# Optimization experiments

Measured on AMD Instinct MI355X. Metric: run time of the kernel, lower is better.

## Reference

```python
import jax, jax.numpy as jnp
import numpy as np

NEG_INF = -1e30
LRELU_SLOPE = 0.2

B, E, IN_DIM, OUT_DIM = 64, 512, 1024, 256


def setup_inputs() -> dict:
    key = jax.random.key(0)
    ks = jax.random.split(key, 6)
    input_state = jax.random.normal(ks[0], (B, E, IN_DIM), dtype=jnp.float32)
    adj = jnp.ones((B, E, E), dtype=jnp.float32)  # only used via ones_like in the original
    node_mask = jax.random.randint(ks[1], (B, E, 1), 0, 2, dtype=jnp.int32)
    W_w = jax.random.normal(ks[2], (OUT_DIM, IN_DIM), dtype=jnp.float32) * (1.0 / np.sqrt(IN_DIM))
    W_b = jax.random.normal(ks[3], (OUT_DIM,), dtype=jnp.float32) * 0.02
    a_w = jax.random.normal(ks[4], (1, 2 * OUT_DIM), dtype=jnp.float32) * (1.0 / np.sqrt(2 * OUT_DIM))
    a_b = jax.random.normal(ks[5], (1,), dtype=jnp.float32) * 0.02
    return {"input_state": input_state, "adj": adj, "node_mask": node_mask,
            "W_w": W_w, "W_b": W_b, "a_w": a_w, "a_b": a_b}


def reference(input_state, adj, node_mask, W_w, W_b, a_w, a_b):
    # h = W(input_state); dropout is identity in eval mode (gnn_drop=0)
    h = jnp.einsum('bei,oi->beo', input_state, W_w) + W_b  # b,E,d
    d = h.shape[-1]
    # a([h_i ; h_j]) decomposes exactly: a_w[:, :d] @ h_i + a_w[:, d:] @ h_j + a_b
    a1, a2 = a_w[:, :d], a_w[:, d:]
    s1 = jnp.einsum('beo,xo->bex', h, a1)  # b,E,1 -> score contribution of source node i
    s2 = jnp.einsum('beo,xo->bex', h, a2)  # b,E,1 -> contribution of target node j
    scores = s1 + jnp.swapaxes(s2, 1, 2) + a_b  # b,E,E, scores[n,i,j] = a([h_i;h_j])
    scores = jnp.where(scores >= 0, scores, LRELU_SLOPE * scores)  # LeakyReLU(0.2)
    # fully-connected adjacency gated by node mask: mask_i * mask_j
    m = node_mask.astype(scores.dtype)  # b,E,1
    pair_mask = m * jnp.swapaxes(m, 1, 2)  # b,E,E
    scores = jnp.where(pair_mask > 0, scores, NEG_INF)
    coefs = jax.nn.softmax(scores, axis=-1)  # b,E,E
    h = h * m  # zero out masked nodes before aggregation
    return jnp.einsum('bij,bjo->bio', coefs, h)
```

## Files before the change

kernel.cpp:

```cpp
#include <hip/hip_runtime.h>
#include <hip/hip_fp16.h>
#include <math.h>

#define NEG_INF_F (-1e30f)
#define LRELU 0.2f

constexpr int Bb = 64, Ee = 512, IND = 1024, OUTD = 256;
constexpr int Mrows = Bb * Ee;

typedef __attribute__((ext_vector_type(8))) _Float16 half8;
typedef __attribute__((ext_vector_type(4))) _Float16 half4;
typedef __attribute__((ext_vector_type(4))) float floatx4;

#define AS1 __attribute__((address_space(1)))
#define AS3 __attribute__((address_space(3)))

__global__ __launch_bounds__(256) void wconv_kernel(
    const float* __restrict__ W, _Float16* __restrict__ Whf)
{
    const int i = (blockIdx.x * 256 + threadIdx.x) * 4;
    const float4 w = *reinterpret_cast<const float4*>(&W[i]);
    half4 hh;
    hh[0] = (_Float16)w.x; hh[1] = (_Float16)w.y;
    hh[2] = (_Float16)w.z; hh[3] = (_Float16)w.w;
    *reinterpret_cast<half4*>(&Whf[i]) = hh;
}

__global__ __launch_bounds__(256, 2) void gemm_h_f16(
    const float* __restrict__ X, const _Float16* __restrict__ Whf,
    const float* __restrict__ Wb, const float* __restrict__ aw,
    const int* __restrict__ mask,
    _Float16* __restrict__ HmTh, float* __restrict__ s1, float* __restrict__ s2)
{
    __shared__ char lds_raw[73728];
    float*    Af  = (float*)lds_raw;
    _Float16* Bf  = (_Float16*)(lds_raw + 24576);
    _Float16* Th   = (_Float16*)lds_raw;
    float*    s1p  = (float*)(lds_raw + 32768);
    float*    s2p  = (float*)(lds_raw + 33792);
    float*    mkfs = (float*)(lds_raw + 34816);

    const int t  = threadIdx.x;
    const int w  = t >> 6, l = t & 63, ln = l & 15, lg = l >> 4;
    const int m0 = blockIdx.x * 64;

    const int arl = l >> 3;
    const int agl = (l & 7) ^ arl;
    const int brl = l >> 2;
    const int bgl = (l & 3) ^ ((l >> 3) & 3);

    floatx4 acc[4][4];
    #pragma unroll
    for (int i = 0; i < 4; ++i)
        #pragma unroll
        for (int j = 0; j < 4; ++j)
            acc[i][j] = (floatx4)0.f;

    auto stageA = [&](int kc, int aoff) {
        #pragma unroll
        for (int i = 0; i < 2; ++i) {
            const int rbase = (w * 2 + i) * 8;
            const size_t src = (size_t)(m0 + rbase + arl) * IND + kc * 32 + agl * 4;
            __builtin_amdgcn_global_load_lds(
                (const AS1 unsigned int*)(X + src),
                (AS3 unsigned int*)(Af + aoff + rbase * 32), 16, 0, 0);
        }
    };
    auto stageB = [&](int kc, int boff) {
        #pragma unroll
        for (int i = 0; i < 4; ++i) {
            const int nbase = w * 64 + i * 16;
            const size_t src = (size_t)(nbase + brl) * IND + kc * 32 + bgl * 8;
            __builtin_amdgcn_global_load_lds(
                (const AS1 unsigned int*)(Whf + src),
                (AS3 unsigned int*)(Bf + boff + nbase * 32), 16, 0, 0);
        }
    };

    int aO0 = 0, aO1 = 2048, aO2 = 4096;
    int bO0 = 0, bO1 = 8192, bO2 = 16384;

    stageA(0, aO0); stageB(0, bO0);
    stageA(1, aO1); stageB(1, bO1);
    asm volatile("s_waitcnt vmcnt(6) lgkmcnt(0)" ::: "memory");
    __builtin_amdgcn_sched_barrier(0);
    __builtin_amdgcn_s_barrier();
    __builtin_amdgcn_sched_barrier(0);

    for (int ts = 0; ts < 32; ++ts) {
        if (ts < 30) { stageA(ts + 2, aO2); stageB(ts + 2, bO2); }
        __builtin_amdgcn_sched_barrier(0);

        half8 bfrag[4];
        #pragma unroll
        for (int nr = 0; nr < 4; ++nr) {
            const int n = w * 64 + nr * 16 + ln;
            const int phys = lg ^ ((n >> 1) & 3);
            bfrag[nr] = *reinterpret_cast<const half8*>(Bf + bO0 + n * 32 + phys * 8);
        }
        half8 afrag[4];
        #pragma unroll
        for (int mr = 0; mr < 4; ++mr) {
            const int r = mr * 16 + ln;
            const int g0 = (lg * 2) ^ (r & 7);
            const int g1 = (lg * 2 + 1) ^ (r & 7);
            const floatx4 a0 = *reinterpret_cast<const floatx4*>(Af + aO0 + r * 32 + g0 * 4);
            const floatx4 a1 = *reinterpret_cast<const floatx4*>(Af + aO0 + r * 32 + g1 * 4);
            half8 h;
            h[0] = (_Float16)a0[0]; h[1] = (_Float16)a0[1];
            h[2] = (_Float16)a0[2]; h[3] = (_Float16)a0[3];
            h[4] = (_Float16)a1[0]; h[5] = (_Float16)a1[1];
            h[6] = (_Float16)a1[2]; h[7] = (_Float16)a1[3];
            afrag[mr] = h;
        }

        __builtin_amdgcn_s_setprio(1);
        #pragma unroll
        for (int mr = 0; mr < 4; ++mr)
            #pragma unroll
            for (int nr = 0; nr < 4; ++nr)
                acc[mr][nr] = __builtin_amdgcn_mfma_f32_16x16x32_f16(
                    afrag[mr], bfrag[nr], acc[mr][nr], 0, 0, 0);
        __builtin_amdgcn_s_setprio(0);

        if (ts < 29) asm volatile("s_waitcnt vmcnt(6) lgkmcnt(0)" ::: "memory");
        else         asm volatile("s_waitcnt vmcnt(0) lgkmcnt(0)" ::: "memory");
        __builtin_amdgcn_sched_barrier(0);
        __builtin_amdgcn_s_barrier();
        __builtin_amdgcn_sched_barrier(0);

        int tmp = aO0; aO0 = aO1; aO1 = aO2; aO2 = tmp;
        tmp = bO0; bO0 = bO1; bO1 = bO2; bO2 = tmp;
    }

    if (t < 64) mkfs[t] = (float)mask[m0 + t];

    float bias[4], a1c[4], a2c[4];
    #pragma unroll
    for (int nr = 0; nr < 4; ++nr) {
        const int n = w * 64 + nr * 16 + ln;
        bias[nr] = Wb[n];
        a1c[nr]  = aw[n];
        a2c[nr]  = aw[OUTD + n];
    }
    float sv1[4][4], sv2[4][4];
    #pragma unroll
    for (int i = 0; i < 4; ++i)
        #pragma unroll
        for (int r = 0; r < 4; ++r) { sv1[i][r] = 0.f; sv2[i][r] = 0.f; }

    #pragma unroll
    for (int mr = 0; mr < 4; ++mr)
        #pragma unroll
        for (int nr = 0; nr < 4; ++nr) {
            const int o = w * 64 + nr * 16 + ln;
            half4 hh;
            #pragma unroll
            for (int rr = 0; rr < 4; ++rr) {
                const float hb = acc[mr][nr][rr] + bias[nr];
                sv1[mr][rr] += hb * a1c[nr];
                sv2[mr][rr] += hb * a2c[nr];
                hh[rr] = (_Float16)hb;
            }
            const int e = mr * 16 + lg * 4;
            *reinterpret_cast<half4*>(Th + o * 64 + (e ^ ((o & 7) << 3))) = hh;
        }

    #pragma unroll
    for (int mr = 0; mr < 4; ++mr)
        #pragma unroll
        for (int rr = 0; rr < 4; ++rr) {
            float v1 = sv1[mr][rr], v2 = sv2[mr][rr];
            #pragma unroll
            for (int off = 1; off < 16; off <<= 1) {
                v1 += __shfl_xor(v1, off, 64);
                v2 += __shfl_xor(v2, off, 64);
            }
            if (ln == 0) {
                const int e = mr * 16 + lg * 4 + rr;
                s1p[w * 64 + e] = v1;
                s2p[w * 64 + e] = v2;
            }
        }
    __syncthreads();

    if (t < 64) {
        s1[m0 + t] = s1p[t] + s1p[64 + t] + s1p[128 + t] + s1p[192 + t];
        s2[m0 + t] = s2p[t] + s2p[64 + t] + s2p[128 + t] + s2p[192 + t];
    }

    const int bIdx = m0 >> 9;
    const int e0   = m0 & 511;
    const int e4   = (t & 15) * 4;
    const float q0 = mkfs[e4 + 0], q1 = mkfs[e4 + 1];
    const float q2 = mkfs[e4 + 2], q3 = mkfs[e4 + 3];
    #pragma unroll
    for (int it = 0; it < 16; ++it) {
        const int o = it * 16 + (t >> 4);
        half4 vh = *reinterpret_cast<const half4*>(Th + o * 64 + (e4 ^ ((o & 7) << 3)));
        if (!(q0 > 0.f)) vh[0] = (_Float16)0.f;
        if (!(q1 > 0.f)) vh[1] = (_Float16)0.f;
        if (!(q2 > 0.f)) vh[2] = (_Float16)0.f;
        if (!(q3 > 0.f)) vh[3] = (_Float16)0.f;
        const size_t goff = ((size_t)(bIdx * OUTD + o) << 9) + e0 + e4;
        *reinterpret_cast<half4*>(&HmTh[goff]) = vh;
    }
}

__global__ __launch_bounds__(256, 2) void attn_mfma(
    const _Float16* __restrict__ HmTh,
    const float* __restrict__ s1, const float* __restrict__ s2,
    const int* __restrict__ mask, const float* __restrict__ ab_ptr,
    float* __restrict__ Out)
{
    __shared__ float s2v[Ee];
    __shared__ float mkv[Ee];
    __shared__ float rowc[64];
    __shared__ float rmax[64];
    __shared__ int   rvv[64];
    __shared__ _Float16 Pl[2][64][32];
    __shared__ float Zp[64][4];
    __shared__ float zr[64];
    __shared__ float wmax[4];

    const int bid = blockIdx.x;
    const int b  = bid & 63;
    const int i0 = (bid >> 6) * 64;
    const int t  = threadIdx.x;
    const int w  = t >> 6, l = t & 63, ln = l & 15, lg = l >> 4;
    const float ab = ab_ptr[0];

    float lmax = -INFINITY;
    #pragma unroll
    for (int q = 0; q < 2; ++q) {
        const int j = t + q * 256;
        const float sv = s2[b * Ee + j];
        const float mv = (float)mask[b * Ee + j];
        s2v[j] = sv; mkv[j] = mv;
        if (mv > 0.f) lmax = fmaxf(lmax, sv);
    }
    #pragma unroll
    for (int off = 32; off; off >>= 1) lmax = fmaxf(lmax, __shfl_xor(lmax, off, 64));
    if (l == 0) wmax[w] = lmax;
    __syncthreads();
    const float s2max = fmaxf(fmaxf(wmax[0], wmax[1]), fmaxf(wmax[2], wmax[3]));
    const int anyvalid = (s2max > -1e37f) ? 1 : 0;
    if (t < 64) {
        const float c = s1[b * Ee + i0 + t] + ab;
        rowc[t] = c;
        const int mi = mask[b * Ee + i0 + t];
        rvv[t] = (mi != 0) & anyvalid;
        const float rm = c + s2max;
        rmax[t] = (rm >= 0.f) ? rm : LRELU * rm;
    }
    __syncthreads();

    const int pi = t >> 2;
    const int pj = (t & 3) * 8;
    const float prc = rowc[pi];
    const float prm = rmax[pi];
    const int   prv = rvv[pi];
    float zacc = 0.f;

    const size_t obase = (size_t)b * OUTD * Ee;
    const int o0 = w * 64;

    floatx4 acc[4][4];
    #pragma unroll
    for (int i = 0; i < 4; ++i)
        #pragma unroll
        for (int j = 0; j < 4; ++j)
            acc[i][j] = (floatx4)0.f;

    for (int ks = 0; ks < 16; ++ks) {
        const int k0  = ks * 32;
        const int buf = ks & 1;

        half8 ph;
        #pragma unroll
        for (int kk = 0; kk < 8; ++kk) {
            const int j = k0 + pj + kk;
            float pv;
            if (prv) {
                float sc = prc + s2v[j];
                sc = (sc >= 0.f) ? sc : LRELU * sc;
                pv = (mkv[j] > 0.f) ? __expf(sc - prm) : 0.f;
            } else {
                pv = 1.f;
            }
            const _Float16 hq = (_Float16)pv;
            ph[kk] = hq;
            zacc += (float)hq;
        }
        *reinterpret_cast<half8*>(&Pl[buf][pi][pj]) = ph;

        half8 bh[4];
        #pragma unroll
        for (int ot = 0; ot < 4; ++ot) {
            const size_t ro = obase + (size_t)(o0 + ot * 16 + ln) * Ee + k0 + lg * 8;
            bh[ot] = *reinterpret_cast<const half8*>(&HmTh[ro]);
        }
        __syncthreads();

        half8 af[4];
        #pragma unroll
        for (int mr = 0; mr < 4; ++mr)
            af[mr] = *reinterpret_cast<const half8*>(&Pl[buf][mr * 16 + ln][lg * 8]);
        #pragma unroll
        for (int mr = 0; mr < 4; ++mr)
            #pragma unroll
            for (int ot = 0; ot < 4; ++ot)
                acc[mr][ot] = __builtin_amdgcn_mfma_f32_16x16x32_f16(
                    af[mr], bh[ot], acc[mr][ot], 0, 0, 0);
    }

    Zp[pi][t & 3] = zacc;
    __syncthreads();
    if (t < 64) {
        const float z = Zp[t][0] + Zp[t][1] + Zp[t][2] + Zp[t][3];
        zr[t] = 1.f / z;
    }
    __syncthreads();

    float* __restrict__ Ob = Out + ((size_t)b * Ee + i0) * OUTD;
    #pragma unroll
    for (int mr = 0; mr < 4; ++mr)
        #pragma unroll
        for (int rr = 0; rr < 4; ++rr) {
            const int i = mr * 16 + lg * 4 + rr;
            const float rzi = zr[i];
            #pragma unroll
            for (int ot = 0; ot < 4; ++ot)
                Ob[(size_t)i * OUTD + o0 + ot * 16 + ln] = acc[mr][ot][rr] * rzi;
        }
}

extern "C" void kernel_launch(void* const* d_in, const int* in_sizes, int n_in,
                              void* d_out, int out_size, void* d_ws, size_t ws_size,
                              hipStream_t stream) {
    const float* X    = (const float*)d_in[0];
    const int*   mask = (const int*)d_in[2];
    const float* Ww   = (const float*)d_in[3];
    const float* Wb   = (const float*)d_in[4];
    const float* aw   = (const float*)d_in[5];
    const float* ab   = (const float*)d_in[6];
    float* out = (float*)d_out;

    _Float16* HmTh = (_Float16*)d_ws;
    float* s1 = (float*)(HmTh + (size_t)Bb * OUTD * Ee);
    float* s2 = s1 + Mrows;
    _Float16* Whf = (_Float16*)(s2 + Mrows);

    wconv_kernel<<<OUTD * IND / (256 * 4), 256, 0, stream>>>(Ww, Whf);
    gemm_h_f16<<<Mrows / 64, 256, 0, stream>>>(X, Whf, Wb, aw, mask, HmTh, s1, s2);
    attn_mfma<<<Bb * (Ee / 64), 256, 0, stream>>>(HmTh, s1, s2, mask, ab, out);
}
```

Baseline: 73.31 us.

## Load GEMM operands directly from global into registers, dropping LDS staging

```diff
diff --git a/kernel.cpp b/kernel.cpp
--- a/kernel.cpp
+++ b/kernel.cpp
@@ -11,9 +11,6 @@
 typedef __attribute__((ext_vector_type(8))) _Float16 half8;
 typedef __attribute__((ext_vector_type(4))) _Float16 half4;
 typedef __attribute__((ext_vector_type(4))) float floatx4;
-
-#define AS1 __attribute__((address_space(1)))
-#define AS3 __attribute__((address_space(3)))
 
 __global__ __launch_bounds__(256) void wconv_kernel(
     const float* __restrict__ W, _Float16* __restrict__ Whf)
@@ -26,15 +23,13 @@
     *reinterpret_cast<half4*>(&Whf[i]) = hh;
 }
 
-__global__ __launch_bounds__(256, 2) void gemm_h_f16(
+__global__ __launch_bounds__(256) void gemm_h_f16(
     const float* __restrict__ X, const _Float16* __restrict__ Whf,
     const float* __restrict__ Wb, const float* __restrict__ aw,
     const int* __restrict__ mask,
     _Float16* __restrict__ HmTh, float* __restrict__ s1, float* __restrict__ s2)
 {
-    __shared__ char lds_raw[73728];
-    float*    Af  = (float*)lds_raw;
-    _Float16* Bf  = (_Float16*)(lds_raw + 24576);
+    __shared__ char lds_raw[35328];
     _Float16* Th   = (_Float16*)lds_raw;
     float*    s1p  = (float*)(lds_raw + 32768);
     float*    s2p  = (float*)(lds_raw + 33792);
@@ -44,10 +39,14 @@
     const int w  = t >> 6, l = t & 63, ln = l & 15, lg = l >> 4;
     const int m0 = blockIdx.x * 64;
 
-    const int arl = l >> 3;
-    const int agl = (l & 7) ^ arl;
-    const int brl = l >> 2;
-    const int bgl = (l & 3) ^ ((l >> 3) & 3);
+    const float* __restrict__ xr[4];
+    const _Float16* __restrict__ br[4];
+    #pragma unroll
+    for (int mr = 0; mr < 4; ++mr)
+        xr[mr] = X + (size_t)(m0 + mr * 16 + ln) * IND + lg * 8;
+    #pragma unroll
+    for (int nr = 0; nr < 4; ++nr)
+        br[nr] = Whf + (size_t)(w * 64 + nr * 16 + ln) * IND + lg * 8;
 
     floatx4 acc[4][4];
     #pragma unroll
@@ -56,81 +55,48 @@
         for (int j = 0; j < 4; ++j)
             acc[i][j] = (floatx4)0.f;
 
-    auto stageA = [&](int kc, int aoff) {
-        #pragma unroll
-        for (int i = 0; i < 2; ++i) {
-            const int rbase = (w * 2 + i) * 8;
-            const size_t src = (size_t)(m0 + rbase + arl) * IND + kc * 32 + agl * 4;
-            __builtin_amdgcn_global_load_lds(
-                (const AS1 unsigned int*)(X + src),
-                (AS3 unsigned int*)(Af + aoff + rbase * 32), 16, 0, 0);
-        }
+    floatx4 A0[4][2], A1[4][2];
+    half8   B0[4],    B1[4];
+
+    auto load = [&](int ks, floatx4 (&Aq)[4][2], half8 (&Bq)[4]) {
+        const int koff = ks * 32;
+        #pragma unroll
+        for (int mr = 0; mr < 4; ++mr) {
+            Aq[mr][0] = *reinterpret_cast<const floatx4*>(xr[mr] + koff);
+            Aq[mr][1] = *reinterpret_cast<const floatx4*>(xr[mr] + koff + 4);
+        }
+        #pragma unroll
+        for (int nr = 0; nr < 4; ++nr)
+            Bq[nr] = *reinterpret_cast<const half8*>(br[nr] + koff);
     };
-    auto stageB = [&](int kc, int boff) {
-        #pragma unroll
-        for (int i = 0; i < 4; ++i) {
-            const int nbase = w * 64 + i * 16;
-            const size_t src = (size_t)(nbase + brl) * IND + kc * 32 + bgl * 8;
-            __builtin_amdgcn_global_load_lds(
-                (const AS1 unsigned int*)(Whf + src),
-                (AS3 unsigned int*)(Bf + boff + nbase * 32), 16, 0, 0);
-        }
-    };
-
-    int aO0 = 0, aO1 = 2048, aO2 = 4096;
-    int bO0 = 0, bO1 = 8192, bO2 = 16384;
-
-    stageA(0, aO0); stageB(0, bO0);
-    stageA(1, aO1); stageB(1, bO1);
-    asm volatile("s_waitcnt vmcnt(6) lgkmcnt(0)" ::: "memory");
-    __builtin_amdgcn_sched_barrier(0);
-    __builtin_amdgcn_s_barrier();
-    __builtin_amdgcn_sched_barrier(0);
-
-    for (int ts = 0; ts < 32; ++ts) {
-        if (ts < 30) { stageA(ts + 2, aO2); stageB(ts + 2, bO2); }
-        __builtin_amdgcn_sched_barrier(0);
-
-        half8 bfrag[4];
-        #pragma unroll
-        for (int nr = 0; nr < 4; ++nr) {
-            const int n = w * 64 + nr * 16 + ln;
-            const int phys = lg ^ ((n >> 1) & 3);
-            bfrag[nr] = *reinterpret_cast<const half8*>(Bf + bO0 + n * 32 + phys * 8);
-        }
-        half8 afrag[4];
+    auto compute = [&](const floatx4 (&Aq)[4][2], const half8 (&Bq)[4]) {
+        half8 af[4];
         #pragma unroll
         for (int mr = 0; mr < 4; ++mr) {
-            const int r = mr * 16 + ln;
-            const int g0 = (lg * 2) ^ (r & 7);
-            const int g1 = (lg * 2 + 1) ^ (r & 7);
-            const floatx4 a0 = *reinterpret_cast<const floatx4*>(Af + aO0 + r * 32 + g0 * 4);
-            const floatx4 a1 = *reinterpret_cast<const floatx4*>(Af + aO0 + r * 32 + g1 * 4);
             half8 h;
-            h[0] = (_Float16)a0[0]; h[1] = (_Float16)a0[1];
-            h[2] = (_Float16)a0[2]; h[3] = (_Float16)a0[3];
-            h[4] = (_Float16)a1[0]; h[5] = (_Float16)a1[1];
-            h[6] = (_Float16)a1[2]; h[7] = (_Float16)a1[3];
-            afrag[mr] = h;
-        }
-
+            h[0] = (_Float16)Aq[mr][0][0]; h[1] = (_Float16)Aq[mr][0][1];
+            h[2] = (_Float16)Aq[mr][0][2]; h[3] = (_Float16)Aq[mr][0][3];
+            h[4] = (_Float16)Aq[mr][1][0]; h[5] = (_Float16)Aq[mr][1][1];
+            h[6] = (_Float16)Aq[mr][1][2]; h[7] = (_Float16)Aq[mr][1][3];
+            af[mr] = h;
+        }
         __builtin_amdgcn_s_setprio(1);
         #pragma unroll
         for (int mr = 0; mr < 4; ++mr)
             #pragma unroll
             for (int nr = 0; nr < 4; ++nr)
                 acc[mr][nr] = __builtin_amdgcn_mfma_f32_16x16x32_f16(
-                    afrag[mr], bfrag[nr], acc[mr][nr], 0, 0, 0);
+                    af[mr], Bq[nr], acc[mr][nr], 0, 0, 0);
         __builtin_amdgcn_s_setprio(0);
-
-        if (ts < 29) asm volatile("s_waitcnt vmcnt(6) lgkmcnt(0)" ::: "memory");
-        else         asm volatile("s_waitcnt vmcnt(0) lgkmcnt(0)" ::: "memory");
-        __builtin_amdgcn_sched_barrier(0);
-        __builtin_amdgcn_s_barrier();
-        __builtin_amdgcn_sched_barrier(0);
-
-        int tmp = aO0; aO0 = aO1; aO1 = aO2; aO2 = tmp;
-        tmp = bO0; bO0 = bO1; bO1 = bO2; bO2 = tmp;
+    };
+
+    load(0, A0, B0);
+    for (int p = 0; p < 16; ++p) {
+        load(2 * p + 1, A1, B1);
+        compute(A0, B0);
+        if (p < 15) load(2 * p + 2, A0, B0);
+        compute(A1, B1);
+        if (p & 1) __builtin_amdgcn_s_barrier();
     }
 
     if (t < 64) mkfs[t] = (float)mask[m0 + t];
```

Result: slower. 129.1 us (+76.2%).

## Split GEMM block across eight waves in a 2x4 grid

Applied to the files above, without the earlier changes.

```diff
diff --git a/kernel.cpp b/kernel.cpp
--- a/kernel.cpp
+++ b/kernel.cpp
@@ -26,7 +26,7 @@
     *reinterpret_cast<half4*>(&Whf[i]) = hh;
 }
 
-__global__ __launch_bounds__(256, 2) void gemm_h_f16(
+__global__ __launch_bounds__(512, 4) void gemm_h_f16(
     const float* __restrict__ X, const _Float16* __restrict__ Whf,
     const float* __restrict__ Wb, const float* __restrict__ aw,
     const int* __restrict__ mask,
@@ -42,6 +42,7 @@
 
     const int t  = threadIdx.x;
     const int w  = t >> 6, l = t & 63, ln = l & 15, lg = l >> 4;
+    const int wr = w >> 2, wc = w & 3;
     const int m0 = blockIdx.x * 64;
 
     const int arl = l >> 3;
@@ -49,27 +50,23 @@
     const int brl = l >> 2;
     const int bgl = (l & 3) ^ ((l >> 3) & 3);
 
-    floatx4 acc[4][4];
-    #pragma unroll
-    for (int i = 0; i < 4; ++i)
+    floatx4 acc[2][4];
+    #pragma unroll
+    for (int i = 0; i < 2; ++i)
         #pragma unroll
         for (int j = 0; j < 4; ++j)
             acc[i][j] = (floatx4)0.f;
 
     auto stageA = [&](int kc, int aoff) {
-        #pragma unroll
-        for (int i = 0; i < 2; ++i) {
-            const int rbase = (w * 2 + i) * 8;
-            const size_t src = (size_t)(m0 + rbase + arl) * IND + kc * 32 + agl * 4;
-            __builtin_amdgcn_global_load_lds(
-                (const AS1 unsigned int*)(X + src),
-                (AS3 unsigned int*)(Af + aoff + rbase * 32), 16, 0, 0);
-        }
+        const size_t src = (size_t)(m0 + w * 8 + arl) * IND + kc * 32 + agl * 4;
+        __builtin_amdgcn_global_load_lds(
+            (const AS1 unsigned int*)(X + src),
+            (AS3 unsigned int*)(Af + aoff + w * 8 * 32), 16, 0, 0);
     };
     auto stageB = [&](int kc, int boff) {
         #pragma unroll
-        for (int i = 0; i < 4; ++i) {
-            const int nbase = w * 64 + i * 16;
+        for (int i = 0; i < 2; ++i) {
+            const int nbase = w * 32 + i * 16;
             const size_t src = (size_t)(nbase + brl) * IND + kc * 32 + bgl * 8;
             __builtin_amdgcn_global_load_lds(
                 (const AS1 unsigned int*)(Whf + src),
@@ -82,7 +79,7 @@
 
     stageA(0, aO0); stageB(0, bO0);
     stageA(1, aO1); stageB(1, bO1);
-    asm volatile("s_waitcnt vmcnt(6) lgkmcnt(0)" ::: "memory");
+    asm volatile("s_waitcnt vmcnt(3) lgkmcnt(0)" ::: "memory");
     __builtin_amdgcn_sched_barrier(0);
     __builtin_amdgcn_s_barrier();
     __builtin_amdgcn_sched_barrier(0);
@@ -94,14 +91,14 @@
         half8 bfrag[4];
         #pragma unroll
         for (int nr = 0; nr < 4; ++nr) {
-            const int n = w * 64 + nr * 16 + ln;
+            const int n = wc * 64 + nr * 16 + ln;
             const int phys = lg ^ ((n >> 1) & 3);
             bfrag[nr] = *reinterpret_cast<const half8*>(Bf + bO0 + n * 32 + phys * 8);
         }
-        half8 afrag[4];
-        #pragma unroll
-        for (int mr = 0; mr < 4; ++mr) {
-            const int r = mr * 16 + ln;
+        half8 afrag[2];
+        #pragma unroll
+        for (int mr = 0; mr < 2; ++mr) {
+            const int r = wr * 32 + mr * 16 + ln;
             const int g0 = (lg * 2) ^ (r & 7);
             const int g1 = (lg * 2 + 1) ^ (r & 7);
             const floatx4 a0 = *reinterpret_cast<const floatx4*>(Af + aO0 + r * 32 + g0 * 4);
@@ -116,14 +113,14 @@
 
         __builtin_amdgcn_s_setprio(1);
         #pragma unroll
-        for (int mr = 0; mr < 4; ++mr)
+        for (int mr = 0; mr < 2; ++mr)
             #pragma unroll
             for (int nr = 0; nr < 4; ++nr)
                 acc[mr][nr] = __builtin_amdgcn_mfma_f32_16x16x32_f16(
                     afrag[mr], bfrag[nr], acc[mr][nr], 0, 0, 0);
         __builtin_amdgcn_s_setprio(0);
 
-        if (ts < 29) asm volatile("s_waitcnt vmcnt(6) lgkmcnt(0)" ::: "memory");
+        if (ts < 30) asm volatile("s_waitcnt vmcnt(3) lgkmcnt(0)" ::: "memory");
         else         asm volatile("s_waitcnt vmcnt(0) lgkmcnt(0)" ::: "memory");
         __builtin_amdgcn_sched_barrier(0);
         __builtin_amdgcn_s_barrier();
@@ -138,22 +135,22 @@
     float bias[4], a1c[4], a2c[4];
     #pragma unroll
     for (int nr = 0; nr < 4; ++nr) {
-        const int n = w * 64 + nr * 16 + ln;
+        const int n = wc * 64 + nr * 16 + ln;
         bias[nr] = Wb[n];
         a1c[nr]  = aw[n];
         a2c[nr]  = aw[OUTD + n];
     }
-    float sv1[4][4], sv2[4][4];
-    #pragma unroll
-    for (int i = 0; i < 4; ++i)
+    float sv1[2][4], sv2[2][4];
+    #pragma unroll
+    for (int i = 0; i < 2; ++i)
         #pragma unroll
         for (int r = 0; r < 4; ++r) { sv1[i][r] = 0.f; sv2[i][r] = 0.f; }
 
     #pragma unroll
-    for (int mr = 0; mr < 4; ++mr)
+    for (int mr = 0; mr < 2; ++mr)
         #pragma unroll
         for (int nr = 0; nr < 4; ++nr) {
-            const int o = w * 64 + nr * 16 + ln;
+            const int o = wc * 64 + nr * 16 + ln;
             half4 hh;
             #pragma unroll
             for (int rr = 0; rr < 4; ++rr) {
@@ -162,12 +159,12 @@
                 sv2[mr][rr] += hb * a2c[nr];
                 hh[rr] = (_Float16)hb;
             }
-            const int e = mr * 16 + lg * 4;
+            const int e = wr * 32 + mr * 16 + lg * 4;
             *reinterpret_cast<half4*>(Th + o * 64 + (e ^ ((o & 7) << 3))) = hh;
         }
 
     #pragma unroll
-    for (int mr = 0; mr < 4; ++mr)
+    for (int mr = 0; mr < 2; ++mr)
         #pragma unroll
         for (int rr = 0; rr < 4; ++rr) {
             float v1 = sv1[mr][rr], v2 = sv2[mr][rr];
@@ -177,16 +174,18 @@
                 v2 += __shfl_xor(v2, off, 64);
             }
             if (ln == 0) {
-                const int e = mr * 16 + lg * 4 + rr;
-                s1p[w * 64 + e] = v1;
-                s2p[w * 64 + e] = v2;
+                const int el = mr * 16 + lg * 4 + rr;
+                s1p[w * 32 + el] = v1;
+                s2p[w * 32 + el] = v2;
             }
         }
     __syncthreads();
 
     if (t < 64) {
-        s1[m0 + t] = s1p[t] + s1p[64 + t] + s1p[128 + t] + s1p[192 + t];
-        s2[m0 + t] = s2p[t] + s2p[64 + t] + s2p[128 + t] + s2p[192 + t];
+        const int wrr = t >> 5, el = t & 31;
+        const int b0 = (wrr * 4) * 32 + el;
+        s1[m0 + t] = s1p[b0] + s1p[b0 + 32] + s1p[b0 + 64] + s1p[b0 + 96];
+        s2[m0 + t] = s2p[b0] + s2p[b0 + 32] + s2p[b0 + 64] + s2p[b0 + 96];
     }
 
     const int bIdx = m0 >> 9;
@@ -195,8 +194,8 @@
     const float q0 = mkfs[e4 + 0], q1 = mkfs[e4 + 1];
     const float q2 = mkfs[e4 + 2], q3 = mkfs[e4 + 3];
     #pragma unroll
-    for (int it = 0; it < 16; ++it) {
-        const int o = it * 16 + (t >> 4);
+    for (int it = 0; it < 8; ++it) {
+        const int o = it * 32 + (t >> 4);
         half4 vh = *reinterpret_cast<const half4*>(Th + o * 64 + (e4 ^ ((o & 7) << 3)));
         if (!(q0 > 0.f)) vh[0] = (_Float16)0.f;
         if (!(q1 > 0.f)) vh[1] = (_Float16)0.f;
@@ -352,6 +351,6 @@
     _Float16* Whf = (_Float16*)(s2 + Mrows);
 
     wconv_kernel<<<OUTD * IND / (256 * 4), 256, 0, stream>>>(Ww, Whf);
-    gemm_h_f16<<<Mrows / 64, 256, 0, stream>>>(X, Whf, Wb, aw, mask, HmTh, s1, s2);
+    gemm_h_f16<<<Mrows / 64, 512, 0, stream>>>(X, Whf, Wb, aw, mask, HmTh, s1, s2);
     attn_mfma<<<Bb * (Ee / 64), 256, 0, stream>>>(HmTh, s1, s2, mask, ab, out);
 }
```

After: 72.83 us. Within noise of the previous version (-0.7%).

## Warp-specialize GEMM with dedicated producer waves for A and B loads

Applied to the files above, without the earlier changes.

```diff
diff --git a/kernel.cpp b/kernel.cpp
--- a/kernel.cpp
+++ b/kernel.cpp
@@ -26,29 +26,24 @@
     *reinterpret_cast<half4*>(&Whf[i]) = hh;
 }
 
-__global__ __launch_bounds__(256, 2) void gemm_h_f16(
+__global__ __launch_bounds__(384, 3) void gemm_h_f16(
     const float* __restrict__ X, const _Float16* __restrict__ Whf,
     const float* __restrict__ Wb, const float* __restrict__ aw,
     const int* __restrict__ mask,
     _Float16* __restrict__ HmTh, float* __restrict__ s1, float* __restrict__ s2)
 {
-    __shared__ char lds_raw[73728];
+    __shared__ char lds_raw[81920];
     float*    Af  = (float*)lds_raw;
-    _Float16* Bf  = (_Float16*)(lds_raw + 24576);
+    _Float16* Bf  = (_Float16*)(lds_raw + 32768);
     _Float16* Th   = (_Float16*)lds_raw;
-    float*    s1p  = (float*)(lds_raw + 32768);
-    float*    s2p  = (float*)(lds_raw + 33792);
-    float*    mkfs = (float*)(lds_raw + 34816);
+    float*    s1p  = (float*)(lds_raw + 65536);
+    float*    s2p  = (float*)(lds_raw + 66560);
+    float*    mkfs = (float*)(lds_raw + 67584);
 
     const int t  = threadIdx.x;
     const int w  = t >> 6, l = t & 63, ln = l & 15, lg = l >> 4;
     const int m0 = blockIdx.x * 64;
 
-    const int arl = l >> 3;
-    const int agl = (l & 7) ^ arl;
-    const int brl = l >> 2;
-    const int bgl = (l & 3) ^ ((l >> 3) & 3);
-
     floatx4 acc[4][4];
     #pragma unroll
     for (int i = 0; i < 4; ++i)
@@ -56,132 +51,159 @@
         for (int j = 0; j < 4; ++j)
             acc[i][j] = (floatx4)0.f;
 
-    auto stageA = [&](int kc, int aoff) {
-        #pragma unroll
-        for (int i = 0; i < 2; ++i) {
-            const int rbase = (w * 2 + i) * 8;
-            const size_t src = (size_t)(m0 + rbase + arl) * IND + kc * 32 + agl * 4;
-            __builtin_amdgcn_global_load_lds(
-                (const AS1 unsigned int*)(X + src),
-                (AS3 unsigned int*)(Af + aoff + rbase * 32), 16, 0, 0);
-        }
-    };
-    auto stageB = [&](int kc, int boff) {
-        #pragma unroll
-        for (int i = 0; i < 4; ++i) {
-            const int nbase = w * 64 + i * 16;
-            const size_t src = (size_t)(nbase + brl) * IND + kc * 32 + bgl * 8;
-            __builtin_amdgcn_global_load_lds(
-                (const AS1 unsigned int*)(Whf + src),
-                (AS3 unsigned int*)(Bf + boff + nbase * 32), 16, 0, 0);
-        }
-    };
-
-    int aO0 = 0, aO1 = 2048, aO2 = 4096;
-    int bO0 = 0, bO1 = 8192, bO2 = 16384;
-
-    stageA(0, aO0); stageB(0, bO0);
-    stageA(1, aO1); stageB(1, bO1);
-    asm volatile("s_waitcnt vmcnt(6) lgkmcnt(0)" ::: "memory");
-    __builtin_amdgcn_sched_barrier(0);
-    __builtin_amdgcn_s_barrier();
-    __builtin_amdgcn_sched_barrier(0);
-
-    for (int ts = 0; ts < 32; ++ts) {
-        if (ts < 30) { stageA(ts + 2, aO2); stageB(ts + 2, bO2); }
+    if (w < 4) {
+        __builtin_amdgcn_s_barrier();
+        for (int ts = 0; ts < 32; ++ts) {
+            __builtin_amdgcn_sched_barrier(0);
+            const int aS = (ts & 3) * 2048;
+            const int bS = (ts % 3) * 8192;
+
+            half8 bfrag[4];
+            #pragma unroll
+            for (int nr = 0; nr < 4; ++nr) {
+                const int n = w * 64 + nr * 16 + ln;
+                const int phys = lg ^ ((n >> 1) & 3);
+                bfrag[nr] = *reinterpret_cast<const half8*>(Bf + bS + n * 32 + phys * 8);
+            }
+            half8 afrag[4];
+            #pragma unroll
+            for (int mr = 0; mr < 4; ++mr) {
+                const int r = mr * 16 + ln;
+                const int g0 = (lg * 2) ^ (r & 7);
+                const int g1 = (lg * 2 + 1) ^ (r & 7);
+                const floatx4 a0 = *reinterpret_cast<const floatx4*>(Af + aS + r * 32 + g0 * 4);
+                const floatx4 a1 = *reinterpret_cast<const floatx4*>(Af + aS + r * 32 + g1 * 4);
+                half8 h;
+                h[0] = (_Float16)a0[0]; h[1] = (_Float16)a0[1];
+                h[2] = (_Float16)a0[2]; h[3] = (_Float16)a0[3];
+                h[4] = (_Float16)a1[0]; h[5] = (_Float16)a1[1];
+                h[6] = (_Float16)a1[2]; h[7] = (_Float16)a1[3];
+                afrag[mr] = h;
+            }
+
+            __builtin_amdgcn_s_setprio(1);
+            #pragma unroll
+            for (int mr = 0; mr < 4; ++mr)
+                #pragma unroll
+                for (int nr = 0; nr < 4; ++nr)
+                    acc[mr][nr] = __builtin_amdgcn_mfma_f32_16x16x32_f16(
+                        afrag[mr], bfrag[nr], acc[mr][nr], 0, 0, 0);
+            __builtin_amdgcn_s_setprio(0);
+            __builtin_amdgcn_sched_barrier(0);
+            __builtin_amdgcn_s_barrier();
+        }
+    } else if (w == 4) {
+        const int arl = l >> 3;
+        const int agl = (l & 7) ^ arl;
+        auto stageA = [&](int kc, int slot) {
+            #pragma unroll
+            for (int i = 0; i < 8; ++i) {
+                const int rbase = i * 8;
+                const size_t src = (size_t)(m0 + rbase + arl) * IND + kc * 32 + agl * 4;
+                __builtin_amdgcn_global_load_lds(
+                    (const AS1 unsigned int*)(X + src),
+                    (AS3 unsigned int*)(Af + slot * 2048 + rbase * 32), 16, 0, 0);
+            }
+        };
+        stageA(0, 0); stageA(1, 1); stageA(2, 2);
+        asm volatile("s_waitcnt vmcnt(16)" ::: "memory");
         __builtin_amdgcn_sched_barrier(0);
-
-        half8 bfrag[4];
+        __builtin_amdgcn_s_barrier();
+        for (int ts = 0; ts < 32; ++ts) {
+            __builtin_amdgcn_sched_barrier(0);
+            if (ts <= 28) {
+                stageA(ts + 3, (ts + 3) & 3);
+                asm volatile("s_waitcnt vmcnt(16)" ::: "memory");
+            } else if (ts == 29) {
+                asm volatile("s_waitcnt vmcnt(8)" ::: "memory");
+            } else if (ts == 30) {
+                asm volatile("s_waitcnt vmcnt(0)" ::: "memory");
+            }
+            __builtin_amdgcn_sched_barrier(0);
+            __builtin_amdgcn_s_barrier();
+        }
+    } else {
+        const int brl = l >> 2;
+        const int bgl = (l & 3) ^ ((l >> 3) & 3);
+        auto stageB = [&](int kc, int slot) {
+            #pragma unroll
+            for (int i = 0; i < 16; ++i) {
+                const int nbase = i * 16;
+                const size_t src = (size_t)(nbase + brl) * IND + kc * 32 + bgl * 8;
+                __builtin_amdgcn_global_load_lds(
+                    (const AS1 unsigned int*)(Whf + src),
+                    (AS3 unsigned int*)(Bf + slot * 8192 + nbase * 32), 16, 0, 0);
+            }
+        };
+        stageB(0, 0); stageB(1, 1);
+        asm volatile("s_waitcnt vmcnt(16)" ::: "memory");
+        __builtin_amdgcn_sched_barrier(0);
+        __builtin_amdgcn_s_barrier();
+        for (int ts = 0; ts < 32; ++ts) {
+            __builtin_amdgcn_sched_barrier(0);
+            if (ts <= 29) {
+                stageB(ts + 2, (ts + 2) % 3);
+                asm volatile("s_waitcnt vmcnt(16)" ::: "memory");
+            } else if (ts == 30) {
+                asm volatile("s_waitcnt vmcnt(0)" ::: "memory");
+            }
+            __builtin_amdgcn_sched_barrier(0);
+            __builtin_amdgcn_s_barrier();
+        }
+    }
+
+    __syncthreads();
+    if (t < 64) mkfs[t] = (float)mask[m0 + t];
+
+    if (t < 256) {
+        float bias[4], a1c[4], a2c[4];
         #pragma unroll
         for (int nr = 0; nr < 4; ++nr) {
             const int n = w * 64 + nr * 16 + ln;
-            const int phys = lg ^ ((n >> 1) & 3);
-            bfrag[nr] = *reinterpret_cast<const half8*>(Bf + bO0 + n * 32 + phys * 8);
-        }
-        half8 afrag[4];
-        #pragma unroll
-        for (int mr = 0; mr < 4; ++mr) {
-            const int r = mr * 16 + ln;
-            const int g0 = (lg * 2) ^ (r & 7);
-            const int g1 = (lg * 2 + 1) ^ (r & 7);
-            const floatx4 a0 = *reinterpret_cast<const floatx4*>(Af + aO0 + r * 32 + g0 * 4);
-            const floatx4 a1 = *reinterpret_cast<const floatx4*>(Af + aO0 + r * 32 + g1 * 4);
-            half8 h;
-            h[0] = (_Float16)a0[0]; h[1] = (_Float16)a0[1];
-            h[2] = (_Float16)a0[2]; h[3] = (_Float16)a0[3];
-            h[4] = (_Float16)a1[0]; h[5] = (_Float16)a1[1];
-            h[6] = (_Float16)a1[2]; h[7] = (_Float16)a1[3];
-            afrag[mr] = h;
-        }
-
-        __builtin_amdgcn_s_setprio(1);
+            bias[nr] = Wb[n];
+            a1c[nr]  = aw[n];
+            a2c[nr]  = aw[OUTD + n];
+        }
+        float sv1[4][4], sv2[4][4];
+        #pragma unroll
+        for (int i = 0; i < 4; ++i)
+            #pragma unroll
+            for (int r = 0; r < 4; ++r) { sv1[i][r] = 0.f; sv2[i][r] = 0.f; }
+
         #pragma unroll
         for (int mr = 0; mr < 4; ++mr)
             #pragma unroll
-            for (int nr = 0; nr < 4; ++nr)
-                acc[mr][nr] = __builtin_amdgcn_mfma_f32_16x16x32_f16(
-                    afrag[mr], bfrag[nr], acc[mr][nr], 0, 0, 0);
-        __builtin_amdgcn_s_setprio(0);
-
-        if (ts < 29) asm volatile("s_waitcnt vmcnt(6) lgkmcnt(0)" ::: "memory");
-        else         asm volatile("s_waitcnt vmcnt(0) lgkmcnt(0)" ::: "memory");
-        __builtin_amdgcn_sched_barrier(0);
-        __builtin_amdgcn_s_barrier();
-        __builtin_amdgcn_sched_barrier(0);
-
-        int tmp = aO0; aO0 = aO1; aO1 = aO2; aO2 = tmp;
-        tmp = bO0; bO0 = bO1; bO1 = bO2; bO2 = tmp;
-    }
-
-    if (t < 64) mkfs[t] = (float)mask[m0 + t];
-
-    float bias[4], a1c[4], a2c[4];
-    #pragma unroll
-    for (int nr = 0; nr < 4; ++nr) {
-        const int n = w * 64 + nr * 16 + ln;
-        bias[nr] = Wb[n];
-        a1c[nr]  = aw[n];
-        a2c[nr]  = aw[OUTD + n];
-    }
-    float sv1[4][4], sv2[4][4];
-    #pragma unroll
-    for (int i = 0; i < 4; ++i)
-        #pragma unroll
-        for (int r = 0; r < 4; ++r) { sv1[i][r] = 0.f; sv2[i][r] = 0.f; }
-
-    #pragma unroll
-    for (int mr = 0; mr < 4; ++mr)
-        #pragma unroll
-        for (int nr = 0; nr < 4; ++nr) {
-            const int o = w * 64 + nr * 16 + ln;
-            half4 hh;
+            for (int nr = 0; nr < 4; ++nr) {
+                const int o = w * 64 + nr * 16 + ln;
+                half4 hh;
+                #pragma unroll
+                for (int rr = 0; rr < 4; ++rr) {
+                    const float hb = acc[mr][nr][rr] + bias[nr];
+                    sv1[mr][rr] += hb * a1c[nr];
+                    sv2[mr][rr] += hb * a2c[nr];
+                    hh[rr] = (_Float16)hb;
+                }
+                const int e = mr * 16 + lg * 4;
+                *reinterpret_cast<half4*>(Th + o * 64 + (e ^ ((o & 7) << 3))) = hh;
+            }
+
+        #pragma unroll
+        for (int mr = 0; mr < 4; ++mr)
             #pragma unroll
             for (int rr = 0; rr < 4; ++rr) {
-                const float hb = acc[mr][nr][rr] + bias[nr];
-                sv1[mr][rr] += hb * a1c[nr];
-                sv2[mr][rr] += hb * a2c[nr];
-                hh[rr] = (_Float16)hb;
-            }
-            const int e = mr * 16 + lg * 4;
-            *reinterpret_cast<half4*>(Th + o * 64 + (e ^ ((o & 7) << 3))) = hh;
-        }
-
-    #pragma unroll
-    for (int mr = 0; mr < 4; ++mr)
-        #pragma unroll
-        for (int rr = 0; rr < 4; ++rr) {
-            float v1 = sv1[mr][rr], v2 = sv2[mr][rr];
-            #pragma unroll
-            for (int off = 1; off < 16; off <<= 1) {
-                v1 += __shfl_xor(v1, off, 64);
-                v2 += __shfl_xor(v2, off, 64);
-            }
-            if (ln == 0) {
-                const int e = mr * 16 + lg * 4 + rr;
-                s1p[w * 64 + e] = v1;
-                s2p[w * 64 + e] = v2;
-            }
-        }
+                float v1 = sv1[mr][rr], v2 = sv2[mr][rr];
+                #pragma unroll
+                for (int off = 1; off < 16; off <<= 1) {
+                    v1 += __shfl_xor(v1, off, 64);
+                    v2 += __shfl_xor(v2, off, 64);
+                }
+                if (ln == 0) {
+                    const int e = mr * 16 + lg * 4 + rr;
+                    s1p[w * 64 + e] = v1;
+                    s2p[w * 64 + e] = v2;
+                }
+            }
+    }
     __syncthreads();
 
     if (t < 64) {
@@ -189,21 +211,23 @@
         s2[m0 + t] = s2p[t] + s2p[64 + t] + s2p[128 + t] + s2p[192 + t];
     }
 
-    const int bIdx = m0 >> 9;
-    const int e0   = m0 & 511;
-    const int e4   = (t & 15) * 4;
-    const float q0 = mkfs[e4 + 0], q1 = mkfs[e4 + 1];
-    const float q2 = mkfs[e4 + 2], q3 = mkfs[e4 + 3];
-    #pragma unroll
-    for (int it = 0; it < 16; ++it) {
-        const int o = it * 16 + (t >> 4);
-        half4 vh = *reinterpret_cast<const half4*>(Th + o * 64 + (e4 ^ ((o & 7) << 3)));
-        if (!(q0 > 0.f)) vh[0] = (_Float16)0.f;
-        if (!(q1 > 0.f)) vh[1] = (_Float16)0.f;
-        if (!(q2 > 0.f)) vh[2] = (_Float16)0.f;
-        if (!(q3 > 0.f)) vh[3] = (_Float16)0.f;
-        const size_t goff = ((size_t)(bIdx * OUTD + o) << 9) + e0 + e4;
-        *reinterpret_cast<half4*>(&HmTh[goff]) = vh;
+    if (t < 256) {
+        const int bIdx = m0 >> 9;
+        const int e0   = m0 & 511;
+        const int e4   = (t & 15) * 4;
+        const float q0 = mkfs[e4 + 0], q1 = mkfs[e4 + 1];
+        const float q2 = mkfs[e4 + 2], q3 = mkfs[e4 + 3];
+        #pragma unroll
+        for (int it = 0; it < 16; ++it) {
+            const int o = it * 16 + (t >> 4);
+            half4 vh = *reinterpret_cast<const half4*>(Th + o * 64 + (e4 ^ ((o & 7) << 3)));
+            if (!(q0 > 0.f)) vh[0] = (_Float16)0.f;
+            if (!(q1 > 0.f)) vh[1] = (_Float16)0.f;
+            if (!(q2 > 0.f)) vh[2] = (_Float16)0.f;
+            if (!(q3 > 0.f)) vh[3] = (_Float16)0.f;
+            const size_t goff = ((size_t)(bIdx * OUTD + o) << 9) + e0 + e4;
+            *reinterpret_cast<half4*>(&HmTh[goff]) = vh;
+        }
     }
 }
 
@@ -352,6 +376,6 @@
     _Float16* Whf = (_Float16*)(s2 + Mrows);
 
     wconv_kernel<<<OUTD * IND / (256 * 4), 256, 0, stream>>>(Ww, Whf);
-    gemm_h_f16<<<Mrows / 64, 256, 0, stream>>>(X, Whf, Wb, aw, mask, HmTh, s1, s2);
+    gemm_h_f16<<<Mrows / 64, 384, 0, stream>>>(X, Whf, Wb, aw, mask, HmTh, s1, s2);
     attn_mfma<<<Bb * (Ee / 64), 256, 0, stream>>>(HmTh, s1, s2, mask, ab, out);
 }
```

Measured after the change: 77.09 us. 5.2% more time.
